# Optimization experiments

Hardware: AMD Instinct MI355X
Metric: run time of the kernel (lower is better)

Reference implementation:

```python
import jax, jax.numpy as jnp
import numpy as np

B, T, D, K = 4, 2048, 1024, 4

def setup_inputs() -> dict:
    key = jax.random.key(0)
    ks = jax.random.split(key, 4)
    u = jax.random.normal(ks[0], (B, T, D), dtype=jnp.float32)
    s0 = jnp.zeros((B, K, D), dtype=jnp.float32)
    W_in = jax.random.normal(ks[1], (K * D, D), dtype=jnp.float32) * (1.0 / np.sqrt(D))
    b_in = jnp.zeros((K * D,), dtype=jnp.float32)
    W_out = jax.random.normal(ks[2], (D, K * D), dtype=jnp.float32) * (1.0 / np.sqrt(K * D))
    b_out = jnp.zeros((D,), dtype=jnp.float32)
    decay_logit = jax.random.normal(ks[3], (K,), dtype=jnp.float32)
    return {"u": u, "s0": s0, "W_in": W_in, "b_in": b_in,
            "W_out": W_out, "b_out": b_out, "decay_logit": decay_logit}

def reference(u, s0, W_in, b_in, W_out, b_out, decay_logit):
    # u: (B,T,D); s0: (B,K,D)
    Bb, Tt, Dd = u.shape
    Kk = decay_logit.shape[0]
    # input projection -> (B,T,K,D) -> (T,B,K,D) for scan over time
    inp = (jnp.einsum('btd,ed->bte', u, W_in) + b_in).reshape(Bb, Tt, Kk, Dd)
    xs = jnp.transpose(inp, (1, 0, 2, 3))  # (T,B,K,D)
    decay = jax.nn.sigmoid(decay_logit).reshape(1, Kk, 1)  # (1,K,1)

    def step(s, x):
        s_next = decay * s + x
        return s_next, s_next

    s_last, s_seq = jax.lax.scan(step, s0, xs)  # s_seq: (T,B,K,D)
    g_in = jnp.transpose(s_seq, (1, 0, 2, 3)).reshape(Bb, Tt, Kk * Dd)
    g = jnp.einsum('bte,de->btd', g_in, W_out) + b_out
    return g, s_last
```

## Files before the change

### kernel.cpp

```cpp
#include <hip/hip_runtime.h>


#define Bb 4
#define Tt 2048
#define Dd 1024
#define Kk 4
#define BT (Bb*Tt)
#define Ee (Kk*Dd)
#define NCH 32
#define LCH 64

typedef __bf16 bf16x8 __attribute__((ext_vector_type(8)));
typedef float  f32x4  __attribute__((ext_vector_type(4)));

__device__ __forceinline__ float bf2f(ushort u){
  union { unsigned int i; float f; } x; x.i = ((unsigned int)u) << 16; return x.f;
}
__device__ __forceinline__ ushort f2bf(float f){
  union { unsigned int i; float f; } x; x.f = f;
  unsigned int i = x.i;
  return (ushort)((i + 0x7FFFu + ((i >> 16) & 1u)) >> 16);
}
__device__ __forceinline__ float lo16(unsigned u){
  union { unsigned i; float f; } x; x.i = u << 16; return x.f;
}
__device__ __forceinline__ float hi16(unsigned u){
  union { unsigned i; float f; } x; x.i = u & 0xFFFF0000u; return x.f;
}
__device__ __forceinline__ float sigm(float x){ return 1.0f / (1.0f + expf(-x)); }

__global__ __launch_bounds__(256) void k_prep_all(
    const float* __restrict__ u, const float* __restrict__ dlog,
    float* __restrict__ vpart, ushort* __restrict__ U_bf,
    const float* __restrict__ W_in, ushort* __restrict__ WinT,
    const float* __restrict__ Wout, const float* __restrict__ s0,
    const float* __restrict__ b_in, ushort* __restrict__ Wout_bf,
    float* __restrict__ z0, float* __restrict__ cterm){
  const int bid = blockIdx.x;
  const int tid = threadIdx.x;

  if (bid < 128){
    int x = bid, c = x & 31, b = x >> 5;
    int d0 = tid * 4;
    float p[4];
    #pragma unroll
    for (int k = 0; k < 4; ++k) p[k] = sigm(dlog[k]);
    f32x4 a0 = {0,0,0,0}, a1 = {0,0,0,0}, a2 = {0,0,0,0}, a3 = {0,0,0,0};
    size_t ub = ((size_t)(b*Tt + c*LCH)) * Dd + d0;
    for (int i = 0; i < LCH; ++i){
      f32x4 uv = *(const f32x4*)(u + ub);
      ushort4 ob; ob.x = f2bf(uv[0]); ob.y = f2bf(uv[1]);
      ob.z = f2bf(uv[2]); ob.w = f2bf(uv[3]);
      *(ushort4*)(U_bf + ub) = ob;
      a0 = p[0]*a0 + uv; a1 = p[1]*a1 + uv; a2 = p[2]*a2 + uv; a3 = p[3]*a3 + uv;
      ub += Dd;
    }
    size_t vb = ((size_t)x * Kk) * Dd + d0;
    *(f32x4*)(vpart + vb)          = a0;
    *(f32x4*)(vpart + vb + Dd)     = a1;
    *(f32x4*)(vpart + vb + 2*Dd)   = a2;
    *(f32x4*)(vpart + vb + 3*Dd)   = a3;
  } else if (bid < 4224){
    __shared__ float tile[32][33];
    int bb = bid - 128;
    int c0 = (bb & 31) * 32, r0 = (bb >> 5) * 32;
    int tx = tid & 31, ty = tid >> 5;
    #pragma unroll
    for (int j = 0; j < 4; ++j)
      tile[ty + j*8][tx] = W_in[(size_t)(r0 + ty + j*8) * Dd + c0 + tx];
    __syncthreads();
    #pragma unroll
    for (int j = 0; j < 4; ++j)
      WinT[(size_t)(c0 + ty + j*8) * Ee + r0 + tx] = f2bf(tile[tx][ty + j*8]);
  } else {
    int gid  = (bid - 4224) * 4 + (tid >> 6);
    int lane = tid & 63;
    int d = gid & 1023, k = gid >> 10;
    const float* wrow = Wout + (size_t)d * Ee + k * Dd;
    ushort*      wbf  = Wout_bf + (size_t)d * Ee + k * Dd;
    const float* bv   = b_in + k * Dd;
    float sc = 0.f, sz0 = 0.f, sz1 = 0.f, sz2 = 0.f, sz3 = 0.f;
    #pragma unroll
    for (int j = 0; j < 4; ++j){
      int base = lane*4 + j*256;
      float4 wv = *(const float4*)(wrow + base);
      ushort4 ob; ob.x = f2bf(wv.x); ob.y = f2bf(wv.y); ob.z = f2bf(wv.z); ob.w = f2bf(wv.w);
      *(ushort4*)(wbf + base) = ob;
      float4 bb4 = *(const float4*)(bv + base);
      sc += wv.x*bb4.x + wv.y*bb4.y + wv.z*bb4.z + wv.w*bb4.w;
      #pragma unroll
      for (int b = 0; b < 4; ++b){
        const float* sv = s0 + ((size_t)(b*Kk + k) << 10) + base;
        float4 s4 = *(const float4*)sv;
        float acc = wv.x*s4.x + wv.y*s4.y + wv.z*s4.z + wv.w*s4.w;
        if (b == 0) sz0 += acc; else if (b == 1) sz1 += acc;
        else if (b == 2) sz2 += acc; else sz3 += acc;
      }
    }
    for (int off = 32; off; off >>= 1){
      sc  += __shfl_down(sc, off);
      sz0 += __shfl_down(sz0, off);
      sz1 += __shfl_down(sz1, off);
      sz2 += __shfl_down(sz2, off);
      sz3 += __shfl_down(sz3, off);
    }
    if (lane == 0){
      cterm[gid] = sc;
      z0[gid]          = sz0;
      z0[gid + 4096]   = sz1;
      z0[gid + 8192]   = sz2;
      z0[gid + 12288]  = sz3;
    }
  }
}

__global__ __launch_bounds__(256) void gemm_nt(const ushort* __restrict__ A,
                                               const ushort* __restrict__ B,
                                               ushort* __restrict__ C,
                                               int Kred, int lda, int ldb, int ldc,
                                               long aBatch, long bBatch, long cBatch){
  __shared__ ushort As[128 * 32];
  __shared__ ushort Bs[128 * 32];
  A += (long)blockIdx.z * aBatch;
  B += (long)blockIdx.z * bBatch;
  C += (long)blockIdx.z * cBatch;
  const int tid  = threadIdx.x;
  const int lane = tid & 63;
  const int w    = tid >> 6;
  const int wr   = w >> 1, wc = w & 1;
  const int rowBase = blockIdx.x * 128;
  const int colBase = blockIdx.y * 128;

  f32x4 acc[4][4] = {};
  const int krow = (lane >> 4) * 8;
  const int rsel = lane & 15;

  for (int kk = 0; kk < Kred; kk += 32){
    __syncthreads();
    #pragma unroll
    for (int i = 0; i < 2; ++i){
      int c  = i * 256 + tid;
      int r  = c >> 2;
      int c8 = (c & 3) * 8;
      const ushort* ga = A + (size_t)(rowBase + r) * lda + kk + c8;
      const ushort* gb = B + (size_t)(colBase + r) * ldb + kk + c8;
      __builtin_amdgcn_global_load_lds((const __attribute__((address_space(1))) void*)ga,
                                       (__attribute__((address_space(3))) void*)&As[c * 8],
                                       16, 0, 0);
      __builtin_amdgcn_global_load_lds((const __attribute__((address_space(1))) void*)gb,
                                       (__attribute__((address_space(3))) void*)&Bs[c * 8],
                                       16, 0, 0);
    }
    asm volatile("s_waitcnt vmcnt(0)" ::: "memory");
    __syncthreads();

    bf16x8 Af[4], Bf[4];
    #pragma unroll
    for (int mi = 0; mi < 4; ++mi)
      Af[mi] = *(const bf16x8*)&As[(wr*64 + mi*16 + rsel) * 32 + krow];
    #pragma unroll
    for (int ni = 0; ni < 4; ++ni)
      Bf[ni] = *(const bf16x8*)&Bs[(wc*64 + ni*16 + rsel) * 32 + krow];
    #pragma unroll
    for (int mi = 0; mi < 4; ++mi)
      #pragma unroll
      for (int ni = 0; ni < 4; ++ni)
        acc[mi][ni] = __builtin_amdgcn_mfma_f32_16x16x32_bf16(Af[mi], Bf[ni], acc[mi][ni], 0, 0, 0);
  }

  #pragma unroll
  for (int mi = 0; mi < 4; ++mi){
    #pragma unroll
    for (int ni = 0; ni < 4; ++ni){
      int r0 = rowBase + wr*64 + mi*16 + (lane >> 4) * 4;
      int c0 = colBase + wc*64 + ni*16 + (lane & 15);
      #pragma unroll
      for (int q = 0; q < 4; ++q)
        C[(size_t)(r0 + q) * ldc + c0] = f2bf(acc[mi][ni][q]);
    }
  }
}

#define STAGE_OP(GB, LOFF)                                                     \
  { _Pragma("unroll")                                                          \
    for (int i_ = 0; i_ < 2; ++i_){                                            \
      int c_ = tid + i_*256;                                                   \
      int row_ = c_ >> 2;                                                      \
      int ss_ = (c_ & 3) ^ ((row_ >> 1) & 3);                                  \
      const ushort* g_ = (GB) + (size_t)row_ * 1024 + ss_ * 8;                 \
      __builtin_amdgcn_global_load_lds(                                        \
        (const __attribute__((address_space(1))) void*)g_,                     \
        (__attribute__((address_space(3))) void*)&lds[(LOFF) + c_*8],          \
        16, 0, 0);                                                             \
    } }

#define LOAD_A4(DST)                                                           \
  { _Pragma("unroll")                                                          \
    for (int mi_ = 0; mi_ < 4; ++mi_){                                         \
      int r_ = wm*64 + mi_*16 + rsel;                                          \
      int uo_ = r_*32 + kq*8;                                                  \
      uo_ ^= ((uo_ >> 6) & 3) << 3;                                            \
      DST[mi_] = *(const bf16x8*)&lds[cbase + uo_];                            \
    } }

#define LOAD_B4(DST)                                                           \
  { _Pragma("unroll")                                                          \
    for (int ni_ = 0; ni_ < 4; ++ni_){                                         \
      int r_ = wn*64 + ni_*16 + rsel;                                          \
      int uo_ = r_*32 + kq*8;                                                  \
      uo_ ^= ((uo_ >> 6) & 3) << 3;                                            \
      DST[ni_] = *(const bf16x8*)&lds[cbase + 4096 + uo_];                     \
    } }

#define XB(R) ((((R) & 3) ^ (((R) >> 2) & 3)) << 5)
#define BAR() __builtin_amdgcn_s_barrier()

__global__ __launch_bounds__(256, 4) void gemm_big(const ushort* __restrict__ A,
                                                   const ushort* __restrict__ B,
                                                   ushort* __restrict__ C,
                                                   const float* __restrict__ dlog,
                                                   float* __restrict__ carry){
  __shared__ ushort lds[16384];
  const int tid  = threadIdx.x;
  const int lane = tid & 63;
  const int w    = tid >> 6;
  const int wm   = w >> 1;
  const int wn   = w & 1;
  const int rsel = lane & 15;
  const int kq   = lane >> 4;

  int bid = blockIdx.x;
  int xcd = bid & 7, rr = bid >> 3;
  const int rowBase = ((xcd >> 1) * 16 + (rr & 15)) * 128;
  const int colBase = ((xcd & 1) * 16 + (rr >> 4)) * 128;

  const ushort* Ag = A + (size_t)rowBase * 1024;
  const ushort* Bg = B + (size_t)colBase * 1024;

  f32x4 acc[4][4] = {};

  STAGE_OP(Ag +  0, 0);
  STAGE_OP(Bg +  0, 4096);
  STAGE_OP(Ag + 32, 8192);
  STAGE_OP(Bg + 32, 8192 + 4096);
  asm volatile("s_waitcnt vmcnt(4)" ::: "memory");
  BAR();

  for (int t = 0; t < 32; ++t){
    const int cbase = (t & 1) * 8192;
    bf16x8 af[4], bf[4];
    LOAD_A4(af); LOAD_B4(bf);
    #pragma unroll
    for (int mi = 0; mi < 4; ++mi)
      #pragma unroll
      for (int ni = 0; ni < 4; ++ni)
        acc[mi][ni] = __builtin_amdgcn_mfma_f32_16x16x32_bf16(af[mi], bf[ni], acc[mi][ni], 0, 0, 0);
    asm volatile("s_waitcnt lgkmcnt(0)" ::: "memory");
    BAR();
    if (t < 30){
      STAGE_OP(Ag + (t+2)*32, cbase);
      STAGE_OP(Bg + (t+2)*32, cbase + 4096);
      asm volatile("s_waitcnt vmcnt(4)" ::: "memory");
    } else {
      asm volatile("s_waitcnt vmcnt(0)" ::: "memory");
    }
    BAR();
  }

  #pragma unroll
  for (int mi = 0; mi < 4; ++mi){
    #pragma unroll
    for (int j = 0; j < 4; ++j){
      #pragma unroll
      for (int q = 0; q < 4; ++q){
        int row = wm*64 + mi*16 + (lane >> 4)*4 + q;
        int col = wn*64 + j*16 + rsel;
        int byte = (row*256 + col*2) ^ XB(row);
        *(ushort*)((char*)lds + byte) = f2bf(acc[mi][j][q]);
      }
    }
  }
  __syncthreads();

  if (tid < 128){
    const int k_blk = colBase >> 10;
    const int b_blk = rowBase >> 11;
    const int ch0   = (rowBase & 2047) >> 6;
    const int d0    = colBase & 1023;
    const float p   = sigm(dlog[k_blk]);
    int cp = tid & 63, ch = tid >> 6;
    float a0 = 0.f, a1 = 0.f;
    for (int i = 0; i < 64; ++i){
      int row = ch*64 + i;
      int byte = (row*256 + cp*4) ^ XB(row);
      unsigned v = *(const unsigned*)((char*)lds + byte);
      a0 = p * a0 + lo16(v);
      a1 = p * a1 + hi16(v);
    }
    float* cdst = &carry[(size_t)((b_blk*Kk + k_blk)*NCH + ch0 + ch) * Dd + d0 + cp*2];
    cdst[0] = a0; cdst[1] = a1;
  }

  #pragma unroll
  for (int j = 0; j < 8; ++j){
    int idx = tid + j*256;
    int r = idx >> 4, c16 = idx & 15;
    int byte = (r*256 + c16*16) ^ XB(r);
    f32x4 v = *(const f32x4*)((char*)lds + byte);
    *(f32x4*)&C[(size_t)(rowBase + r) * Ee + colBase + c16*8] = v;
  }
}

__global__ __launch_bounds__(256) void k_mid(const float* __restrict__ carry,
                                             const float* __restrict__ z0,
                                             const float* __restrict__ dlog,
                                             float* __restrict__ incoming,
                                             const float* __restrict__ vpart,
                                             float* __restrict__ vfull){
  int bid = blockIdx.x, tid = threadIdx.x;
  if (bid < 64){
    int idx = bid * 256 + tid;
    int k = (idx >> 10) & 3;
    int bk = idx >> 10, d = idx & 1023;
    float p  = sigm(dlog[k]);
    float dL = powf(p, (float)LCH);
    float inc = z0[idx];
    for (int c = 0; c < NCH; ++c){
      size_t o = ((size_t)(bk * NCH + c)) * Dd + d;
      incoming[o] = inc;
      inc = dL * inc + carry[o];
    }
  } else {
    int idx = (bid - 64) * 256 + tid;
    int k = (idx >> 10) & 3, b = idx >> 12, d = idx & 1023;
    float p  = sigm(dlog[k]);
    float dL = powf(p, (float)LCH);
    float v = 0.f;
    for (int c = 0; c < NCH; ++c)
      v = dL * v + vpart[(((size_t)(b*NCH + c)) * Kk + k) * Dd + d];
    vfull[idx] = v;
  }
}

__global__ __launch_bounds__(256) void k_final(const ushort* __restrict__ Y,
                                               const float* __restrict__ incoming,
                                               const float* __restrict__ dlog,
                                               const float* __restrict__ b_out,
                                               const float* __restrict__ cterm,
                                               float* __restrict__ g,
                                               const float* __restrict__ W_in,
                                               const float* __restrict__ vfull,
                                               const float* __restrict__ s0,
                                               const float* __restrict__ b_in,
                                               float* __restrict__ slast){
  int bid = blockIdx.x, tid = threadIdx.x;
  if (bid < 256){
    int x = bid >> 1;
    int c = x & 31, b = x >> 5;
    int d = (bid & 1) * 512 + tid * 2;
    float p[4], ct0[4], ct1[4], pw[4];
    float z0v[4], z1v[4];
    #pragma unroll
    for (int k = 0; k < 4; ++k){
      p[k]  = sigm(dlog[k]);
      size_t io = ((size_t)(((b*Kk + k))*NCH + c)) * Dd + d;
      z0v[k] = incoming[io];
      z1v[k] = incoming[io + 1];
      float omp = fmaxf(1.0f - p[k], 1e-30f);
      ct0[k] = cterm[k * Dd + d] / omp;
      ct1[k] = cterm[k * Dd + d + 1] / omp;
      pw[k] = powf(p[k], (float)(c * LCH + 1));
    }
    float bo0 = b_out[d], bo1 = b_out[d + 1];
    size_t ybase = ((size_t)(b*Tt + c*LCH)) * Ee + d;
    size_t gbase = ((size_t)(b*Tt + c*LCH)) * Dd + d;
    for (int i = 0; i < LCH; ++i){
      float acc0 = bo0, acc1 = bo1;
      #pragma unroll
      for (int k = 0; k < 4; ++k){
        unsigned yv = *(const unsigned*)&Y[ybase + (size_t)k * Dd];
        z0v[k] = p[k] * z0v[k] + lo16(yv);
        z1v[k] = p[k] * z1v[k] + hi16(yv);
        float omw = 1.0f - pw[k];
        acc0 += z0v[k] + ct0[k] * omw;
        acc1 += z1v[k] + ct1[k] * omw;
        pw[k] *= p[k];
      }
      *(float2*)&g[gbase] = make_float2(acc0, acc1);
      ybase += Ee; gbase += Dd;
    }
  } else {
    int gid  = (bid - 256) * 4 + (tid >> 6);
    int lane = tid & 63;
    int d = gid & 1023, k = (gid >> 10) & 3, b = gid >> 12;
    const float* wrow = W_in + (size_t)(k*Dd + d) * Dd;
    const float* vv   = vfull + ((size_t)(b*Kk + k) << 10);
    float s = 0.f;
    #pragma unroll
    for (int j = 0; j < 4; ++j){
      int base = lane*4 + j*256;
      float4 w4 = *(const float4*)(wrow + base);
      float4 v4 = *(const float4*)(vv + base);
      s += w4.x*v4.x + w4.y*v4.y + w4.z*v4.z + w4.w*v4.w;
    }
    for (int off = 32; off; off >>= 1) s += __shfl_down(s, off);
    if (lane == 0){
      float p  = sigm(dlog[k]);
      float pT = powf(p, (float)Tt);
      float omp = 1.0f - p;
      float geo = (omp < 1e-12f) ? (float)Tt : (1.0f - pT) / omp;
      slast[gid] = pT * s0[gid] + s + b_in[k*Dd + d] * geo;
    }
  }
}

extern "C" void kernel_launch(void* const* d_in, const int* in_sizes, int n_in,
                              void* d_out, int out_size, void* d_ws, size_t ws_size,
                              hipStream_t stream){
  const float* u     = (const float*)d_in[0];
  const float* s0    = (const float*)d_in[1];
  const float* W_in  = (const float*)d_in[2];
  const float* b_in  = (const float*)d_in[3];
  const float* W_out = (const float*)d_in[4];
  const float* b_out = (const float*)d_in[5];
  const float* dlog  = (const float*)d_in[6];

  float* g_out     = (float*)d_out;
  float* slast_out = g_out + (size_t)BT * Dd;

  char* ws = (char*)d_ws;
  if (ws_size < 115490816ull) return;
  ushort* U_bf    = (ushort*)(ws);
  ushort* WinT    = (ushort*)(ws + 16777216);
  ushort* Wout_bf = (ushort*)(ws + 25165824);
  ushort* Mcat    = (ushort*)(ws + 33554432);
  ushort* Y       = (ushort*)(ws + 41943040);
  float*  carry   = (float*)(ws + 109051904);
  float*  incoming= (float*)(ws + 111149056);
  float*  z0buf   = (float*)(ws + 113246208);
  float*  cterm   = (float*)(ws + 113311744);
  float*  vpart   = (float*)(ws + 113328128);
  float*  vfull   = (float*)(ws + 115425280);

  k_prep_all<<<5248, 256, 0, stream>>>(u, dlog, vpart, U_bf,
                                       W_in, WinT,
                                       W_out, s0, b_in, Wout_bf, z0buf, cterm);

  gemm_nt<<<dim3(8, 8, 4), 256, 0, stream>>>(Wout_bf, WinT, Mcat,
                                             1024, Ee, Ee, Dd,
                                             1024L, 1024L, 1048576L);
  gemm_big<<<2048, 256, 0, stream>>>(U_bf, Mcat, Y, dlog, carry);

  k_mid<<<128, 256, 0, stream>>>(carry, z0buf, dlog, incoming, vpart, vfull);

  k_final<<<4352, 256, 0, stream>>>(Y, incoming, dlog, b_out, cterm, g_out,
                                    W_in, vfull, s0, b_in, slast_out);
}
```

Baseline: 155.0 us.

## Scan raw input before the projection and fuse the output epilogue into the GEMM

The decay scan now runs on the raw input u, since the recurrence is linear and commutes with the input projection. It produces a bf16 zeta tensor of shape (BT, K*D), and one GEMM with K=4096 against the concatenated per-k W_out·W_in product then writes g directly. This removes the intermediate Y tensor, the carry pass and the separate final recurrence kernel, and moves the bias, cterm and s0-decay corrections into the GEMM epilogue. In exchange the big GEMM has a reduction dimension four times longer over fewer output tiles (512 blocks), and the 64 MB zeta tensor must be written to and read back from memory.

```diff
diff --git a/kernel.cpp b/kernel.cpp
--- a/kernel.cpp
+++ b/kernel.cpp
@@ -21,17 +21,11 @@
   unsigned int i = x.i;
   return (ushort)((i + 0x7FFFu + ((i >> 16) & 1u)) >> 16);
 }
-__device__ __forceinline__ float lo16(unsigned u){
-  union { unsigned i; float f; } x; x.i = u << 16; return x.f;
-}
-__device__ __forceinline__ float hi16(unsigned u){
-  union { unsigned i; float f; } x; x.i = u & 0xFFFF0000u; return x.f;
-}
 __device__ __forceinline__ float sigm(float x){ return 1.0f / (1.0f + expf(-x)); }
 
 __global__ __launch_bounds__(256) void k_prep_all(
     const float* __restrict__ u, const float* __restrict__ dlog,
-    float* __restrict__ vpart, ushort* __restrict__ U_bf,
+    float* __restrict__ vpart,
     const float* __restrict__ W_in, ushort* __restrict__ WinT,
     const float* __restrict__ Wout, const float* __restrict__ s0,
     const float* __restrict__ b_in, ushort* __restrict__ Wout_bf,
@@ -49,9 +43,6 @@
     size_t ub = ((size_t)(b*Tt + c*LCH)) * Dd + d0;
     for (int i = 0; i < LCH; ++i){
       f32x4 uv = *(const f32x4*)(u + ub);
-      ushort4 ob; ob.x = f2bf(uv[0]); ob.y = f2bf(uv[1]);
-      ob.z = f2bf(uv[2]); ob.w = f2bf(uv[3]);
-      *(ushort4*)(U_bf + ub) = ob;
       a0 = p[0]*a0 + uv; a1 = p[1]*a1 + uv; a2 = p[2]*a2 + uv; a3 = p[3]*a3 + uv;
       ub += Dd;
     }
@@ -111,6 +102,44 @@
       z0[gid + 8192]   = sz2;
       z0[gid + 12288]  = sz3;
     }
+  }
+}
+
+__global__ __launch_bounds__(256) void k_mid(const float* __restrict__ vpart,
+                                             const float* __restrict__ dlog,
+                                             float* __restrict__ incoming,
+                                             float* __restrict__ vfull){
+  int idx = blockIdx.x * 256 + threadIdx.x;
+  int k = (idx >> 10) & 3, b = idx >> 12, d = idx & 1023;
+  float p  = sigm(dlog[k]);
+  float dL = powf(p, (float)LCH);
+  float inc = 0.f;
+  for (int c = 0; c < NCH; ++c){
+    size_t o = (((size_t)(b*NCH + c)) * Kk + k) * Dd + d;
+    incoming[o] = inc;
+    inc = dL * inc + vpart[o];
+  }
+  vfull[idx] = inc;
+}
+
+__global__ __launch_bounds__(256) void k_zeta(const float* __restrict__ u,
+                                              const float* __restrict__ incoming,
+                                              const float* __restrict__ dlog,
+                                              ushort* __restrict__ zeta){
+  int x = blockIdx.x;
+  int k = blockIdx.y;
+  int c = x & 31, b = x >> 5;
+  int d0 = threadIdx.x * 4;
+  float p = sigm(dlog[k]);
+  f32x4 z = *(const f32x4*)&incoming[(((size_t)x) * Kk + k) * Dd + d0];
+  size_t ub = ((size_t)(b*Tt + c*LCH)) * Dd + d0;
+  size_t zb = ((size_t)(b*Tt + c*LCH)) * Ee + k*Dd + d0;
+  for (int i = 0; i < LCH; ++i){
+    f32x4 uv = *(const f32x4*)(u + ub);
+    z = p*z + uv;
+    ushort4 o; o.x = f2bf(z[0]); o.y = f2bf(z[1]); o.z = f2bf(z[2]); o.w = f2bf(z[3]);
+    *(ushort4*)(zeta + zb) = o;
+    ub += Dd; zb += Ee;
   }
 }
 
@@ -187,7 +216,7 @@
       int c_ = tid + i_*256;                                                   \
       int row_ = c_ >> 2;                                                      \
       int ss_ = (c_ & 3) ^ ((row_ >> 1) & 3);                                  \
-      const ushort* g_ = (GB) + (size_t)row_ * 1024 + ss_ * 8;                 \
+      const ushort* g_ = (GB) + (size_t)row_ * 4096 + ss_ * 8;                 \
       __builtin_amdgcn_global_load_lds(                                        \
         (const __attribute__((address_space(1))) void*)g_,                     \
         (__attribute__((address_space(3))) void*)&lds[(LOFF) + c_*8],          \
@@ -212,14 +241,15 @@
       DST[ni_] = *(const bf16x8*)&lds[cbase + 4096 + uo_];                     \
     } }
 
-#define XB(R) ((((R) & 3) ^ (((R) >> 2) & 3)) << 5)
 #define BAR() __builtin_amdgcn_s_barrier()
 
 __global__ __launch_bounds__(256, 4) void gemm_big(const ushort* __restrict__ A,
                                                    const ushort* __restrict__ B,
-                                                   ushort* __restrict__ C,
+                                                   float* __restrict__ g,
                                                    const float* __restrict__ dlog,
-                                                   float* __restrict__ carry){
+                                                   const float* __restrict__ z0,
+                                                   const float* __restrict__ cterm,
+                                                   const float* __restrict__ b_out){
   __shared__ ushort lds[16384];
   const int tid  = threadIdx.x;
   const int lane = tid & 63;
@@ -231,11 +261,11 @@
 
   int bid = blockIdx.x;
   int xcd = bid & 7, rr = bid >> 3;
-  const int rowBase = ((xcd >> 1) * 16 + (rr & 15)) * 128;
-  const int colBase = ((xcd & 1) * 16 + (rr >> 4)) * 128;
-
-  const ushort* Ag = A + (size_t)rowBase * 1024;
-  const ushort* Bg = B + (size_t)colBase * 1024;
+  const int rowBase = (xcd * 8 + (rr & 7)) * 128;
+  const int colBase = (rr >> 3) * 128;
+
+  const ushort* Ag = A + (size_t)rowBase * 4096;
+  const ushort* Bg = B + (size_t)colBase * 4096;
 
   f32x4 acc[4][4] = {};
 
@@ -246,7 +276,7 @@
   asm volatile("s_waitcnt vmcnt(4)" ::: "memory");
   BAR();
 
-  for (int t = 0; t < 32; ++t){
+  for (int t = 0; t < 128; ++t){
     const int cbase = (t & 1) * 8192;
     bf16x8 af[4], bf[4];
     LOAD_A4(af); LOAD_B4(bf);
@@ -257,7 +287,7 @@
         acc[mi][ni] = __builtin_amdgcn_mfma_f32_16x16x32_bf16(af[mi], bf[ni], acc[mi][ni], 0, 0, 0);
     asm volatile("s_waitcnt lgkmcnt(0)" ::: "memory");
     BAR();
-    if (t < 30){
+    if (t < 126){
       STAGE_OP(Ag + (t+2)*32, cbase);
       STAGE_OP(Bg + (t+2)*32, cbase + 4096);
       asm volatile("s_waitcnt vmcnt(4)" ::: "memory");
@@ -267,150 +297,84 @@
     BAR();
   }
 
-  #pragma unroll
-  for (int mi = 0; mi < 4; ++mi){
+  {
+    const int b  = rowBase >> 11;
+    const int t0 = rowBase & 2047;
+    const int c0 = colBase + wn*64 + rsel;
+    float boj[4], ctsum[4], d0v[4][4];
     #pragma unroll
     for (int j = 0; j < 4; ++j){
+      int cj = c0 + j*16;
+      boj[j] = b_out[cj];
+      float cs = 0.f;
+      #pragma unroll
+      for (int k = 0; k < 4; ++k){
+        float p   = sigm(dlog[k]);
+        float omp = fmaxf(1.0f - p, 1e-30f);
+        float ct  = cterm[k*Dd + cj] / omp;
+        d0v[k][j] = z0[b*4096 + k*Dd + cj] - ct;
+        cs += ct;
+      }
+      ctsum[j] = cs;
+    }
+    float pk[4], p16[4], pwm[4];
+    int tfirst = t0 + wm*64 + (lane >> 4)*4;
+    #pragma unroll
+    for (int k = 0; k < 4; ++k){
+      pk[k]  = sigm(dlog[k]);
+      pwm[k] = powf(pk[k], (float)(tfirst + 1));
+      p16[k] = powf(pk[k], 16.0f);
+    }
+    #pragma unroll
+    for (int mi = 0; mi < 4; ++mi){
+      float pwr[4];
+      #pragma unroll
+      for (int k = 0; k < 4; ++k) pwr[k] = pwm[k];
       #pragma unroll
       for (int q = 0; q < 4; ++q){
-        int row = wm*64 + mi*16 + (lane >> 4)*4 + q;
-        int col = wn*64 + j*16 + rsel;
-        int byte = (row*256 + col*2) ^ XB(row);
-        *(ushort*)((char*)lds + byte) = f2bf(acc[mi][j][q]);
+        int r = rowBase + wm*64 + mi*16 + (lane >> 4)*4 + q;
+        #pragma unroll
+        for (int j = 0; j < 4; ++j){
+          float gg = acc[mi][j][q] + boj[j] + ctsum[j];
+          #pragma unroll
+          for (int k = 0; k < 4; ++k) gg += pwr[k] * d0v[k][j];
+          g[(size_t)r * Dd + c0 + j*16] = gg;
+        }
+        #pragma unroll
+        for (int k = 0; k < 4; ++k) pwr[k] *= pk[k];
       }
-    }
-  }
-  __syncthreads();
-
-  if (tid < 128){
-    const int k_blk = colBase >> 10;
-    const int b_blk = rowBase >> 11;
-    const int ch0   = (rowBase & 2047) >> 6;
-    const int d0    = colBase & 1023;
-    const float p   = sigm(dlog[k_blk]);
-    int cp = tid & 63, ch = tid >> 6;
-    float a0 = 0.f, a1 = 0.f;
-    for (int i = 0; i < 64; ++i){
-      int row = ch*64 + i;
-      int byte = (row*256 + cp*4) ^ XB(row);
-      unsigned v = *(const unsigned*)((char*)lds + byte);
-      a0 = p * a0 + lo16(v);
-      a1 = p * a1 + hi16(v);
-    }
-    float* cdst = &carry[(size_t)((b_blk*Kk + k_blk)*NCH + ch0 + ch) * Dd + d0 + cp*2];
-    cdst[0] = a0; cdst[1] = a1;
-  }
-
-  #pragma unroll
-  for (int j = 0; j < 8; ++j){
-    int idx = tid + j*256;
-    int r = idx >> 4, c16 = idx & 15;
-    int byte = (r*256 + c16*16) ^ XB(r);
-    f32x4 v = *(const f32x4*)((char*)lds + byte);
-    *(f32x4*)&C[(size_t)(rowBase + r) * Ee + colBase + c16*8] = v;
-  }
-}
-
-__global__ __launch_bounds__(256) void k_mid(const float* __restrict__ carry,
-                                             const float* __restrict__ z0,
-                                             const float* __restrict__ dlog,
-                                             float* __restrict__ incoming,
-                                             const float* __restrict__ vpart,
-                                             float* __restrict__ vfull){
-  int bid = blockIdx.x, tid = threadIdx.x;
-  if (bid < 64){
-    int idx = bid * 256 + tid;
-    int k = (idx >> 10) & 3;
-    int bk = idx >> 10, d = idx & 1023;
-    float p  = sigm(dlog[k]);
-    float dL = powf(p, (float)LCH);
-    float inc = z0[idx];
-    for (int c = 0; c < NCH; ++c){
-      size_t o = ((size_t)(bk * NCH + c)) * Dd + d;
-      incoming[o] = inc;
-      inc = dL * inc + carry[o];
-    }
-  } else {
-    int idx = (bid - 64) * 256 + tid;
-    int k = (idx >> 10) & 3, b = idx >> 12, d = idx & 1023;
-    float p  = sigm(dlog[k]);
-    float dL = powf(p, (float)LCH);
-    float v = 0.f;
-    for (int c = 0; c < NCH; ++c)
-      v = dL * v + vpart[(((size_t)(b*NCH + c)) * Kk + k) * Dd + d];
-    vfull[idx] = v;
-  }
-}
-
-__global__ __launch_bounds__(256) void k_final(const ushort* __restrict__ Y,
-                                               const float* __restrict__ incoming,
-                                               const float* __restrict__ dlog,
-                                               const float* __restrict__ b_out,
-                                               const float* __restrict__ cterm,
-                                               float* __restrict__ g,
-                                               const float* __restrict__ W_in,
+      #pragma unroll
+      for (int k = 0; k < 4; ++k) pwm[k] *= p16[k];
+    }
+  }
+}
+
+__global__ __launch_bounds__(256) void k_slast(const float* __restrict__ W_in,
                                                const float* __restrict__ vfull,
                                                const float* __restrict__ s0,
                                                const float* __restrict__ b_in,
-                                               float* __restrict__ slast){
-  int bid = blockIdx.x, tid = threadIdx.x;
-  if (bid < 256){
-    int x = bid >> 1;
-    int c = x & 31, b = x >> 5;
-    int d = (bid & 1) * 512 + tid * 2;
-    float p[4], ct0[4], ct1[4], pw[4];
-    float z0v[4], z1v[4];
-    #pragma unroll
-    for (int k = 0; k < 4; ++k){
-      p[k]  = sigm(dlog[k]);
-      size_t io = ((size_t)(((b*Kk + k))*NCH + c)) * Dd + d;
-      z0v[k] = incoming[io];
-      z1v[k] = incoming[io + 1];
-      float omp = fmaxf(1.0f - p[k], 1e-30f);
-      ct0[k] = cterm[k * Dd + d] / omp;
-      ct1[k] = cterm[k * Dd + d + 1] / omp;
-      pw[k] = powf(p[k], (float)(c * LCH + 1));
-    }
-    float bo0 = b_out[d], bo1 = b_out[d + 1];
-    size_t ybase = ((size_t)(b*Tt + c*LCH)) * Ee + d;
-    size_t gbase = ((size_t)(b*Tt + c*LCH)) * Dd + d;
-    for (int i = 0; i < LCH; ++i){
-      float acc0 = bo0, acc1 = bo1;
-      #pragma unroll
-      for (int k = 0; k < 4; ++k){
-        unsigned yv = *(const unsigned*)&Y[ybase + (size_t)k * Dd];
-        z0v[k] = p[k] * z0v[k] + lo16(yv);
-        z1v[k] = p[k] * z1v[k] + hi16(yv);
-        float omw = 1.0f - pw[k];
-        acc0 += z0v[k] + ct0[k] * omw;
-        acc1 += z1v[k] + ct1[k] * omw;
-        pw[k] *= p[k];
-      }
-      *(float2*)&g[gbase] = make_float2(acc0, acc1);
-      ybase += Ee; gbase += Dd;
-    }
-  } else {
-    int gid  = (bid - 256) * 4 + (tid >> 6);
-    int lane = tid & 63;
-    int d = gid & 1023, k = (gid >> 10) & 3, b = gid >> 12;
-    const float* wrow = W_in + (size_t)(k*Dd + d) * Dd;
-    const float* vv   = vfull + ((size_t)(b*Kk + k) << 10);
-    float s = 0.f;
-    #pragma unroll
-    for (int j = 0; j < 4; ++j){
-      int base = lane*4 + j*256;
-      float4 w4 = *(const float4*)(wrow + base);
-      float4 v4 = *(const float4*)(vv + base);
-      s += w4.x*v4.x + w4.y*v4.y + w4.z*v4.z + w4.w*v4.w;
-    }
-    for (int off = 32; off; off >>= 1) s += __shfl_down(s, off);
-    if (lane == 0){
-      float p  = sigm(dlog[k]);
-      float pT = powf(p, (float)Tt);
-      float omp = 1.0f - p;
-      float geo = (omp < 1e-12f) ? (float)Tt : (1.0f - pT) / omp;
-      slast[gid] = pT * s0[gid] + s + b_in[k*Dd + d] * geo;
-    }
+                                               const float* __restrict__ dlog,
+                                               float* __restrict__ out){
+  int gid  = blockIdx.x * 4 + (threadIdx.x >> 6);
+  int lane = threadIdx.x & 63;
+  int d = gid & 1023, k = (gid >> 10) & 3, b = gid >> 12;
+  const float* wrow = W_in + (size_t)(k*Dd + d) * Dd;
+  const float* vv   = vfull + ((size_t)(b*Kk + k) << 10);
+  float s = 0.f;
+  #pragma unroll
+  for (int j = 0; j < 4; ++j){
+    int base = lane*4 + j*256;
+    float4 w4 = *(const float4*)(wrow + base);
+    float4 v4 = *(const float4*)(vv + base);
+    s += w4.x*v4.x + w4.y*v4.y + w4.z*v4.z + w4.w*v4.w;
+  }
+  for (int off = 32; off; off >>= 1) s += __shfl_down(s, off);
+  if (lane == 0){
+    float p  = sigm(dlog[k]);
+    float pT = powf(p, (float)Tt);
+    float omp = 1.0f - p;
+    float geo = (omp < 1e-12f) ? (float)Tt : (1.0f - pT) / omp;
+    out[gid] = pT * s0[gid] + s + b_in[k*Dd + d] * geo;
   }
 }
 
@@ -430,29 +394,30 @@
 
   char* ws = (char*)d_ws;
   if (ws_size < 115490816ull) return;
-  ushort* U_bf    = (ushort*)(ws);
   ushort* WinT    = (ushort*)(ws + 16777216);
   ushort* Wout_bf = (ushort*)(ws + 25165824);
-  ushort* Mcat    = (ushort*)(ws + 33554432);
-  ushort* Y       = (ushort*)(ws + 41943040);
-  float*  carry   = (float*)(ws + 109051904);
+  ushort* Mcat3   = (ushort*)(ws + 33554432);
+  ushort* zeta    = (ushort*)(ws + 41943040);
   float*  incoming= (float*)(ws + 111149056);
   float*  z0buf   = (float*)(ws + 113246208);
   float*  cterm   = (float*)(ws + 113311744);
   float*  vpart   = (float*)(ws + 113328128);
   float*  vfull   = (float*)(ws + 115425280);
 
-  k_prep_all<<<5248, 256, 0, stream>>>(u, dlog, vpart, U_bf,
+  k_prep_all<<<5248, 256, 0, stream>>>(u, dlog, vpart,
                                        W_in, WinT,
                                        W_out, s0, b_in, Wout_bf, z0buf, cterm);
 
-  gemm_nt<<<dim3(8, 8, 4), 256, 0, stream>>>(Wout_bf, WinT, Mcat,
-                                             1024, Ee, Ee, Dd,
-                                             1024L, 1024L, 1048576L);
-  gemm_big<<<2048, 256, 0, stream>>>(U_bf, Mcat, Y, dlog, carry);
-
-  k_mid<<<128, 256, 0, stream>>>(carry, z0buf, dlog, incoming, vpart, vfull);
-
-  k_final<<<4352, 256, 0, stream>>>(Y, incoming, dlog, b_out, cterm, g_out,
-                                    W_in, vfull, s0, b_in, slast_out);
-}
+  k_mid<<<64, 256, 0, stream>>>(vpart, dlog, incoming, vfull);
+
+  k_zeta<<<dim3(128, 4), 256, 0, stream>>>(u, incoming, dlog, zeta);
+
+  gemm_nt<<<dim3(8, 8, 4), 256, 0, stream>>>(Wout_bf, WinT, Mcat3,
+                                             1024, Ee, Ee, Ee,
+                                             1024L, 1024L, 1024L);
+
+  gemm_big<<<512, 256, 0, stream>>>(zeta, Mcat3, g_out, dlog,
+                                    z0buf, cterm, b_out);
+
+  k_slast<<<4096, 256, 0, stream>>>(W_in, vfull, s0, b_in, dlog, slast_out);
+}
```

Measured after the change: 158.0 us. No clear change (+1.9%).

## Widen gemm_big tile to 128x256 with 4x8 MFMA accumulators per wave

Applied to the files above, without the earlier changes.

Doubles the N dimension of the big GEMM tile so each wave computes a 64x128 output block, halving the block count and the number of A reloads per output. The epilogue is split into two 128-column halves that reuse the LDS staging for the carry scan and the output store. More accumulator registers and LDS reduce occupancy (launch bounds go from 4 to 2 blocks), and the tile-to-XCD mapping changes.

```diff
diff --git a/kernel.cpp b/kernel.cpp
--- a/kernel.cpp
+++ b/kernel.cpp
@@ -181,7 +181,7 @@
   }
 }
 
-#define STAGE_OP(GB, LOFF)                                                     \
+#define STAGE_A(GB, LOFF)                                                      \
   { _Pragma("unroll")                                                          \
     for (int i_ = 0; i_ < 2; ++i_){                                            \
       int c_ = tid + i_*256;                                                   \
@@ -194,6 +194,19 @@
         16, 0, 0);                                                             \
     } }
 
+#define STAGE_B(GB, LOFF)                                                      \
+  { _Pragma("unroll")                                                          \
+    for (int i_ = 0; i_ < 4; ++i_){                                            \
+      int c_ = tid + i_*256;                                                   \
+      int row_ = c_ >> 2;                                                      \
+      int ss_ = (c_ & 3) ^ ((row_ >> 1) & 3);                                  \
+      const ushort* g_ = (GB) + (size_t)row_ * 1024 + ss_ * 8;                 \
+      __builtin_amdgcn_global_load_lds(                                        \
+        (const __attribute__((address_space(1))) void*)g_,                     \
+        (__attribute__((address_space(3))) void*)&lds[(LOFF) + 4096 + c_*8],   \
+        16, 0, 0);                                                             \
+    } }
+
 #define LOAD_A4(DST)                                                           \
   { _Pragma("unroll")                                                          \
     for (int mi_ = 0; mi_ < 4; ++mi_){                                         \
@@ -203,10 +216,10 @@
       DST[mi_] = *(const bf16x8*)&lds[cbase + uo_];                            \
     } }
 
-#define LOAD_B4(DST)                                                           \
+#define LOAD_B8(DST)                                                           \
   { _Pragma("unroll")                                                          \
-    for (int ni_ = 0; ni_ < 4; ++ni_){                                         \
-      int r_ = wn*64 + ni_*16 + rsel;                                          \
+    for (int ni_ = 0; ni_ < 8; ++ni_){                                         \
+      int r_ = wn*128 + ni_*16 + rsel;                                         \
       int uo_ = r_*32 + kq*8;                                                  \
       uo_ ^= ((uo_ >> 6) & 3) << 3;                                            \
       DST[ni_] = *(const bf16x8*)&lds[cbase + 4096 + uo_];                     \
@@ -215,12 +228,12 @@
 #define XB(R) ((((R) & 3) ^ (((R) >> 2) & 3)) << 5)
 #define BAR() __builtin_amdgcn_s_barrier()
 
-__global__ __launch_bounds__(256, 4) void gemm_big(const ushort* __restrict__ A,
+__global__ __launch_bounds__(256, 2) void gemm_big(const ushort* __restrict__ A,
                                                    const ushort* __restrict__ B,
                                                    ushort* __restrict__ C,
                                                    const float* __restrict__ dlog,
                                                    float* __restrict__ carry){
-  __shared__ ushort lds[16384];
+  __shared__ ushort lds[24576];
   const int tid  = threadIdx.x;
   const int lane = tid & 63;
   const int w    = tid >> 6;
@@ -231,36 +244,36 @@
 
   int bid = blockIdx.x;
   int xcd = bid & 7, rr = bid >> 3;
-  const int rowBase = ((xcd >> 1) * 16 + (rr & 15)) * 128;
-  const int colBase = ((xcd & 1) * 16 + (rr >> 4)) * 128;
+  const int rowBase = (xcd * 8 + (rr & 7)) * 128;
+  const int colBase = (rr >> 3) * 256;
 
   const ushort* Ag = A + (size_t)rowBase * 1024;
   const ushort* Bg = B + (size_t)colBase * 1024;
 
-  f32x4 acc[4][4] = {};
-
-  STAGE_OP(Ag +  0, 0);
-  STAGE_OP(Bg +  0, 4096);
-  STAGE_OP(Ag + 32, 8192);
-  STAGE_OP(Bg + 32, 8192 + 4096);
-  asm volatile("s_waitcnt vmcnt(4)" ::: "memory");
+  f32x4 acc[4][8] = {};
+
+  STAGE_A(Ag +  0, 0);
+  STAGE_B(Bg +  0, 0);
+  STAGE_A(Ag + 32, 12288);
+  STAGE_B(Bg + 32, 12288);
+  asm volatile("s_waitcnt vmcnt(6)" ::: "memory");
   BAR();
 
   for (int t = 0; t < 32; ++t){
-    const int cbase = (t & 1) * 8192;
-    bf16x8 af[4], bf[4];
-    LOAD_A4(af); LOAD_B4(bf);
+    const int cbase = (t & 1) * 12288;
+    bf16x8 af[4], bf[8];
+    LOAD_A4(af); LOAD_B8(bf);
     #pragma unroll
     for (int mi = 0; mi < 4; ++mi)
       #pragma unroll
-      for (int ni = 0; ni < 4; ++ni)
+      for (int ni = 0; ni < 8; ++ni)
         acc[mi][ni] = __builtin_amdgcn_mfma_f32_16x16x32_bf16(af[mi], bf[ni], acc[mi][ni], 0, 0, 0);
     asm volatile("s_waitcnt lgkmcnt(0)" ::: "memory");
     BAR();
     if (t < 30){
-      STAGE_OP(Ag + (t+2)*32, cbase);
-      STAGE_OP(Bg + (t+2)*32, cbase + 4096);
-      asm volatile("s_waitcnt vmcnt(4)" ::: "memory");
+      STAGE_A(Ag + (t+2)*32, cbase);
+      STAGE_B(Bg + (t+2)*32, cbase);
+      asm volatile("s_waitcnt vmcnt(6)" ::: "memory");
     } else {
       asm volatile("s_waitcnt vmcnt(0)" ::: "memory");
     }
@@ -268,46 +281,53 @@
   }
 
   #pragma unroll
-  for (int mi = 0; mi < 4; ++mi){
-    #pragma unroll
-    for (int j = 0; j < 4; ++j){
-      #pragma unroll
-      for (int q = 0; q < 4; ++q){
-        int row = wm*64 + mi*16 + (lane >> 4)*4 + q;
-        int col = wn*64 + j*16 + rsel;
-        int byte = (row*256 + col*2) ^ XB(row);
-        *(ushort*)((char*)lds + byte) = f2bf(acc[mi][j][q]);
+  for (int h = 0; h < 2; ++h){
+    if (wn == h){
+      #pragma unroll
+      for (int mi = 0; mi < 4; ++mi){
+        #pragma unroll
+        for (int ni = 0; ni < 8; ++ni){
+          #pragma unroll
+          for (int q = 0; q < 4; ++q){
+            int row = wm*64 + mi*16 + (lane >> 4)*4 + q;
+            int col = ni*16 + rsel;
+            int byte = (row*256 + col*2) ^ XB(row);
+            *(ushort*)((char*)lds + byte) = f2bf(acc[mi][ni][q]);
+          }
+        }
       }
     }
-  }
-  __syncthreads();
-
-  if (tid < 128){
-    const int k_blk = colBase >> 10;
-    const int b_blk = rowBase >> 11;
-    const int ch0   = (rowBase & 2047) >> 6;
-    const int d0    = colBase & 1023;
-    const float p   = sigm(dlog[k_blk]);
-    int cp = tid & 63, ch = tid >> 6;
-    float a0 = 0.f, a1 = 0.f;
-    for (int i = 0; i < 64; ++i){
-      int row = ch*64 + i;
-      int byte = (row*256 + cp*4) ^ XB(row);
-      unsigned v = *(const unsigned*)((char*)lds + byte);
-      a0 = p * a0 + lo16(v);
-      a1 = p * a1 + hi16(v);
-    }
-    float* cdst = &carry[(size_t)((b_blk*Kk + k_blk)*NCH + ch0 + ch) * Dd + d0 + cp*2];
-    cdst[0] = a0; cdst[1] = a1;
-  }
-
-  #pragma unroll
-  for (int j = 0; j < 8; ++j){
-    int idx = tid + j*256;
-    int r = idx >> 4, c16 = idx & 15;
-    int byte = (r*256 + c16*16) ^ XB(r);
-    f32x4 v = *(const f32x4*)((char*)lds + byte);
-    *(f32x4*)&C[(size_t)(rowBase + r) * Ee + colBase + c16*8] = v;
+    __syncthreads();
+
+    const int colH = colBase + h*128;
+    if (tid < 128){
+      const int k_blk = colH >> 10;
+      const int b_blk = rowBase >> 11;
+      const int ch0   = (rowBase & 2047) >> 6;
+      const int d0    = colH & 1023;
+      const float p   = sigm(dlog[k_blk]);
+      int cp = tid & 63, ch = tid >> 6;
+      float a0 = 0.f, a1 = 0.f;
+      for (int i = 0; i < 64; ++i){
+        int row = ch*64 + i;
+        int byte = (row*256 + cp*4) ^ XB(row);
+        unsigned v = *(const unsigned*)((char*)lds + byte);
+        a0 = p * a0 + lo16(v);
+        a1 = p * a1 + hi16(v);
+      }
+      float* cdst = &carry[(size_t)((b_blk*Kk + k_blk)*NCH + ch0 + ch) * Dd + d0 + cp*2];
+      cdst[0] = a0; cdst[1] = a1;
+    }
+
+    #pragma unroll
+    for (int j = 0; j < 8; ++j){
+      int idx = tid + j*256;
+      int r = idx >> 4, c16 = idx & 15;
+      int byte = (r*256 + c16*16) ^ XB(r);
+      f32x4 v = *(const f32x4*)((char*)lds + byte);
+      *(f32x4*)&C[(size_t)(rowBase + r) * Ee + colH + c16*8] = v;
+    }
+    __syncthreads();
   }
 }
 
@@ -449,7 +469,7 @@
   gemm_nt<<<dim3(8, 8, 4), 256, 0, stream>>>(Wout_bf, WinT, Mcat,
                                              1024, Ee, Ee, Dd,
                                              1024L, 1024L, 1048576L);
-  gemm_big<<<2048, 256, 0, stream>>>(U_bf, Mcat, Y, dlog, carry);
+  gemm_big<<<1024, 256, 0, stream>>>(U_bf, Mcat, Y, dlog, carry);
 
   k_mid<<<128, 256, 0, stream>>>(carry, z0buf, dlog, incoming, vpart, vfull);
 
```

Result: no change. 153.3 us (-1.0%).
